# Kernel tuning notes

Hardware: AMD Instinct MI355X
Metric: run time of the kernel (lower is better)

The kernel has to match this reference:

```python
import jax, jax.numpy as jnp
import numpy as np

B, S, D = 2, 2048, 4096
NQ, NKV, DK = 32, 4, 128
GROUPS = NQ // NKV  # 8
NEG = -1e9  # finite stand-in for -inf so fully-masked rows stay NaN-free


def setup_inputs() -> dict:
    key = jax.random.key(0)
    ks = jax.random.split(key, 5)
    return {
        "x": jax.random.normal(ks[0], (B, S, D), jnp.float32),
        "Wq": jax.random.normal(ks[1], (D, NQ * DK), jnp.float32) * 0.02,
        "Wk": jax.random.normal(ks[2], (D, NKV * DK), jnp.float32) * 0.02,
        "Wv": jax.random.normal(ks[3], (D, NKV * DK), jnp.float32) * 0.02,
        "Wo": jax.random.normal(ks[4], (NQ * DK, D), jnp.float32) * 0.02,
    }


def reference(x, Wq, Wk, Wv, Wo):
    b, s, _ = x.shape
    # projections -> [b, heads, s, dk]
    Q = (x @ Wq).reshape(b, s, NQ, DK).transpose(0, 2, 1, 3)
    K = (x @ Wk).reshape(b, s, NKV, DK).transpose(0, 2, 1, 3)
    V = (x @ Wv).reshape(b, s, NKV, DK).transpose(0, 2, 1, 3)
    # GQA: repeat_interleave KV heads to match Q heads
    K = jnp.repeat(K, GROUPS, axis=1)  # [b, NQ, s, dk]
    V = jnp.repeat(V, GROUPS, axis=1)
    scores = jnp.einsum("bhqd,bhkd->bhqk", Q, K) / np.sqrt(DK).astype(np.float32)
    # faithful to source: mask = triu(ones(s, kv_len), diag=kv_len-s+1); fill where mask==0
    mask = jnp.triu(jnp.ones((s, s), jnp.float32), k=1)
    scores = jnp.where(mask == 0, NEG, scores)
    attn = jax.nn.softmax(scores, axis=-1)  # dropout = identity (eval)
    out = jnp.einsum("bhqk,bhkd->bhqd", attn, V)
    out = out.transpose(0, 2, 1, 3).reshape(b, s, NQ * DK)
    return out @ Wo
```

## Files before the change

### kernel.cpp

```cpp
#include <hip/hip_runtime.h>
#include <hip/hip_bf16.h>

#define S_LEN 2048
#define DMODEL 4096
#define NQH 32
#define NKVH 4
#define DKH 128

typedef __attribute__((ext_vector_type(8))) short bf16x8;
typedef __attribute__((ext_vector_type(4))) float f32x4;
typedef __attribute__((ext_vector_type(16))) float f32x16;
typedef __attribute__((ext_vector_type(2))) unsigned u32x2;

union PU { unsigned u[4]; bf16x8 v; };

__device__ __forceinline__ float b2f(short u) {
  union { float f; unsigned int i; } cv;
  cv.i = ((unsigned int)(unsigned short)u) << 16;
  return cv.f;
}

__device__ __forceinline__ unsigned cvt_pk(float lo, float hi) {
  unsigned r;
  asm("v_cvt_pk_bf16_f32 %0, %1, %2" : "=v"(r) : "v"(lo), "v"(hi));
  return r;
}

__device__ __forceinline__ void gload16(const void* g, void* l) {
  __builtin_amdgcn_global_load_lds(
      (const __attribute__((address_space(1))) void*)g,
      (__attribute__((address_space(3))) void*)l, 16, 0, 0);
}

#define BAR()                         \
  {                                   \
    asm volatile("" ::: "memory");    \
    __builtin_amdgcn_s_barrier();     \
    asm volatile("" ::: "memory");    \
  }

__global__ __launch_bounds__(256) void cast_kernel(
    const float* __restrict__ in, __hip_bfloat16* __restrict__ out, int n4) {
  for (int i = blockIdx.x * 256 + threadIdx.x; i < n4; i += gridDim.x * 256) {
    const float4 v = reinterpret_cast<const float4*>(in)[i];
    __hip_bfloat16 t[4] = {__float2bfloat16(v.x), __float2bfloat16(v.y),
                           __float2bfloat16(v.z), __float2bfloat16(v.w)};
    reinterpret_cast<uint2*>(out)[i] = *reinterpret_cast<const uint2*>(t);
  }
}

__device__ __forceinline__ void transpose_tile(const float* __restrict__ W,
                                               __hip_bfloat16* __restrict__ WT,
                                               int K, int N, int n0, int k0,
                                               int tid,
                                               __hip_bfloat16 (*tile)[64]) {
#pragma unroll
  for (int i = 0; i < 2; ++i) {
    const int fid = i * 256 + tid;
    const int r = fid >> 3, cc = fid & 7;
    const float4 v0 = *reinterpret_cast<const float4*>(
        &W[(size_t)(k0 + r) * N + n0 + cc * 8]);
    const float4 v1 = *reinterpret_cast<const float4*>(
        &W[(size_t)(k0 + r) * N + n0 + cc * 8 + 4]);
    __hip_bfloat16 t[8] = {__float2bfloat16(v0.x), __float2bfloat16(v0.y),
                           __float2bfloat16(v0.z), __float2bfloat16(v0.w),
                           __float2bfloat16(v1.x), __float2bfloat16(v1.y),
                           __float2bfloat16(v1.z), __float2bfloat16(v1.w)};
    *reinterpret_cast<bf16x8*>(&tile[r][(cc ^ (r & 7)) << 3]) =
        *reinterpret_cast<const bf16x8*>(t);
  }
  __syncthreads();
  const int n = tid >> 2, kw = tid & 3;
#pragma unroll
  for (int i = 0; i < 2; ++i) {
    const int kc = kw + i * 4;
    __hip_bfloat16 t[8];
#pragma unroll
    for (int j = 0; j < 8; ++j) {
      const int r = kc * 8 + j;
      t[j] = tile[r][((((n >> 3) ^ (r & 7)) << 3)) + (n & 7)];
    }
    *reinterpret_cast<bf16x8*>(&WT[(size_t)(n0 + n) * K + k0 + kc * 8]) =
        *reinterpret_cast<const bf16x8*>(t);
  }
}

__global__ __launch_bounds__(256) void transpose_cast_kernel(
    const float* __restrict__ W, __hip_bfloat16* __restrict__ WT, int K, int N) {
  __shared__ __align__(16) __hip_bfloat16 tile[64][64];
  transpose_tile(W, WT, K, N, blockIdx.x * 64, blockIdx.y * 64, threadIdx.x,
                 tile);
}

__global__ __launch_bounds__(256) void transpose_kv_kernel(
    const float* __restrict__ Wk, const float* __restrict__ Wv,
    __hip_bfloat16* __restrict__ KVT) {
  __shared__ __align__(16) __hip_bfloat16 tile[64][64];
  const int half = blockIdx.x >> 3;
  const float* W = half ? Wv : Wk;
  __hip_bfloat16* WT = KVT + (size_t)half * 512 * 4096;
  transpose_tile(W, WT, 4096, 512, (blockIdx.x & 7) * 64, blockIdx.y * 64,
                 threadIdx.x, tile);
}

template <int WMODE>
__global__ __launch_bounds__(512, 2) void gemm256(
    const __hip_bfloat16* __restrict__ A, const __hip_bfloat16* __restrict__ BT,
    void* __restrict__ C) {
  __shared__ __align__(16) char ldsA[131072];
  const char* lds = &ldsA[0];
  const int tid = threadIdx.x, lane = tid & 63, w = tid >> 6;
  const int l15 = lane & 15, g = lane >> 4;
  const int wr = w >> 2, wcn = w & 3;
  const int id = blockIdx.x;
  const int swz = (id & 7) * 32 + (id >> 3);
  const int bm = (swz >> 4) * 256, bn = (swz & 15) * 256;
  const int row0 = tid >> 3;
  const int kbg = ((tid & 7) * 16) ^ ((row0 & 7) << 4);
  const char* Ab = (const char*)A;
  const char* Bb = (const char*)BT;
  const size_t aR = (size_t)(bm + row0) * 8192 + kbg;
  const size_t bR = (size_t)(bn + row0) * 8192 + kbg;
  char* ldsw = const_cast<char*>(lds) + w * 1024;
  const int sw = (l15 & 7) << 4;
  const int okk = (g * 16) ^ sw;
  const int rA = (wr * 64 + l15) * 128;
  const int rB = (wcn * 32 + l15) * 128;

  f32x4 acc[8][4] = {};

#define STG2(XR, XB, DST)            \
  gload16(XB + (XR), ldsw + (DST));  \
  gload16(XB + (XR) + 524288, ldsw + (DST) + 8192)

  STG2(aR, Ab, 0);
  STG2(bR, Bb, 65536);
  STG2(aR + 1048576, Ab, 16384);
  STG2(bR + 1048576, Bb, 65536 + 16384);
  STG2(aR + 128, Ab, 32768);
  STG2(bR + 128, Bb, 65536 + 32768);

  for (int t = 0; t < 64; ++t) {
    const int pc = t & 1, pn = pc ^ 1;
    const int pA = pc * 32768, pB = 65536 + pc * 32768;
    const size_t s01 = (size_t)((t + 1 < 64) ? t + 1 : t - 1) * 128;
    const size_t s23 = (size_t)((t + 2 < 64) ? t + 2 : t) * 128;
    asm volatile("s_waitcnt vmcnt(4)" ::: "memory");
    BAR();
    bf16x8 a0[4][2], b0[2][2];
#pragma unroll
    for (int m = 0; m < 4; ++m)
#pragma unroll
      for (int kk = 0; kk < 2; ++kk)
        a0[m][kk] = *reinterpret_cast<const bf16x8*>(
            lds + pA + rA + m * 2048 + (okk ^ (kk << 6)));
#pragma unroll
    for (int n = 0; n < 2; ++n)
#pragma unroll
      for (int kk = 0; kk < 2; ++kk)
        b0[n][kk] = *reinterpret_cast<const bf16x8*>(
            lds + pB + rB + n * 2048 + (okk ^ (kk << 6)));
    STG2(aR + 1048576 + s01, Ab, pn * 32768 + 16384);
    __builtin_amdgcn_s_setprio(1);
#pragma unroll
    for (int kk = 0; kk < 2; ++kk)
#pragma unroll
      for (int m = 0; m < 4; ++m)
#pragma unroll
        for (int n = 0; n < 2; ++n)
          acc[m][n] = __builtin_amdgcn_mfma_f32_16x16x32_bf16(
              a0[m][kk], b0[n][kk], acc[m][n], 0, 0, 0);
    __builtin_amdgcn_s_setprio(0);
    bf16x8 b1[2][2];
#pragma unroll
    for (int n = 0; n < 2; ++n)
#pragma unroll
      for (int kk = 0; kk < 2; ++kk)
        b1[n][kk] = *reinterpret_cast<const bf16x8*>(
            lds + pB + 16384 + rB + n * 2048 + (okk ^ (kk << 6)));
    STG2(bR + 1048576 + s01, Bb, 65536 + pn * 32768 + 16384);
    BAR();
    __builtin_amdgcn_s_setprio(1);
#pragma unroll
    for (int kk = 0; kk < 2; ++kk)
#pragma unroll
      for (int m = 0; m < 4; ++m)
#pragma unroll
        for (int n = 0; n < 2; ++n)
          acc[m][2 + n] = __builtin_amdgcn_mfma_f32_16x16x32_bf16(
              a0[m][kk], b1[n][kk], acc[m][2 + n], 0, 0, 0);
    __builtin_amdgcn_s_setprio(0);
    bf16x8 a1[4][2];
#pragma unroll
    for (int m = 0; m < 4; ++m)
#pragma unroll
      for (int kk = 0; kk < 2; ++kk)
        a1[m][kk] = *reinterpret_cast<const bf16x8*>(
            lds + pA + 16384 + rA + m * 2048 + (okk ^ (kk << 6)));
    STG2(aR + s23, Ab, pc * 32768);
    __builtin_amdgcn_s_setprio(1);
#pragma unroll
    for (int kk = 0; kk < 2; ++kk)
#pragma unroll
      for (int m = 0; m < 4; ++m)
#pragma unroll
        for (int n = 0; n < 2; ++n)
          acc[4 + m][n] = __builtin_amdgcn_mfma_f32_16x16x32_bf16(
              a1[m][kk], b0[n][kk], acc[4 + m][n], 0, 0, 0);
    __builtin_amdgcn_s_setprio(0);
    STG2(bR + s23, Bb, 65536 + pc * 32768);
    __builtin_amdgcn_s_setprio(1);
#pragma unroll
    for (int kk = 0; kk < 2; ++kk)
#pragma unroll
      for (int m = 0; m < 4; ++m)
#pragma unroll
        for (int n = 0; n < 2; ++n)
          acc[4 + m][2 + n] = __builtin_amdgcn_mfma_f32_16x16x32_bf16(
              a1[m][kk], b1[n][kk], acc[4 + m][2 + n], 0, 0, 0);
    __builtin_amdgcn_s_setprio(0);
  }
  asm volatile("s_waitcnt vmcnt(0)" ::: "memory");

  const int crow0 = bm + wr * 64 + g * 4;
  const int ccol0 = bn + wcn * 32 + l15;
#pragma unroll
  for (int M = 0; M < 8; ++M)
#pragma unroll
    for (int N = 0; N < 4; ++N) {
      const int row = crow0 + (M >> 2) * 128 + (M & 3) * 16;
      const int col = ccol0 + (N >> 1) * 128 + (N & 1) * 16;
#pragma unroll
      for (int r = 0; r < 4; ++r) {
        if constexpr (WMODE == 0)
          ((float*)C)[(size_t)(row + r) * 4096 + col] = acc[M][N][r];
        else
          ((__hip_bfloat16*)C)[(size_t)(row + r) * 4096 + col] =
              __float2bfloat16(acc[M][N][r]);
      }
    }
}

__global__ __launch_bounds__(256) void gemm_kv(
    const __hip_bfloat16* __restrict__ A, const __hip_bfloat16* __restrict__ BT,
    __hip_bfloat16* __restrict__ Kb, __hip_bfloat16* __restrict__ VT) {
  __shared__ __align__(16) char ldsb[3][12288];
  char* ldsbase = &ldsb[0][0];
  const int tid = threadIdx.x, lane = tid & 63, w = tid >> 6;
  const int l15 = lane & 15, l4 = lane >> 4;
  const int bm = blockIdx.y * 64, bn = blockIdx.x * 128;
  const int wr = (w >> 1) * 32, wc = (w & 1) * 64;
  const int srow = lane >> 2, scol = (lane & 3) * 8;
  const char* ga = (const char*)&A[(size_t)(bm + (tid >> 2)) * 4096 + scol];
  const char* gb =
      (const char*)&BT[(size_t)(bn + w * 16 + srow) * 4096 + scol];
  f32x4 acc[2][4] = {};

#define KVSTG(T, BUF)                                                   \
  {                                                                     \
    const size_t ko = (size_t)(T) * 64;                                 \
    gload16(ga + ko, ldsbase + (BUF) * 12288 + w * 1024);               \
    gload16(gb + ko, ldsbase + (BUF) * 12288 + 4096 + w * 1024);        \
    gload16(gb + 524288 + ko, ldsbase + (BUF) * 12288 + 8192 + w * 1024); \
  }

  KVSTG(0, 0);
  KVSTG(1, 1);
  int cur = 0;
  for (int t = 0; t < 128; ++t) {
    asm volatile("s_waitcnt vmcnt(3)" ::: "memory");
    BAR();
    const char* bp = ldsbase + cur * 12288;
    bf16x8 af[2], bfr[4];
#pragma unroll
    for (int m = 0; m < 2; ++m)
      af[m] = *reinterpret_cast<const bf16x8*>(
          bp + (wr + m * 16 + l15) * 64 + l4 * 16);
#pragma unroll
    for (int n = 0; n < 4; ++n)
      bfr[n] = *reinterpret_cast<const bf16x8*>(
          bp + 4096 + (wc + n * 16 + l15) * 64 + l4 * 16);
    const int t2 = (t + 2 < 128) ? t + 2 : t;
    int b2 = cur + 2;
    if (b2 >= 3) b2 -= 3;
    KVSTG(t2, b2);
#pragma unroll
    for (int m = 0; m < 2; ++m)
#pragma unroll
      for (int n = 0; n < 4; ++n)
        acc[m][n] = __builtin_amdgcn_mfma_f32_16x16x32_bf16(af[m], bfr[n],
                                                            acc[m][n], 0, 0, 0);
    ++cur;
    if (cur == 3) cur = 0;
  }
  asm volatile("s_waitcnt vmcnt(0)" ::: "memory");

#pragma unroll
  for (int m = 0; m < 2; ++m)
#pragma unroll
    for (int n = 0; n < 4; ++n) {
      const int row = bm + wr + m * 16 + l4 * 4;
      const int col = bn + wc + n * 16 + l15;
      if (col < 512) {
#pragma unroll
        for (int r = 0; r < 4; ++r)
          Kb[(size_t)(row + r) * 512 + col] = __float2bfloat16(acc[m][n][r]);
      } else {
        const int b = row >> 11, s = row & 2047;
        uint2 st;
        st.x = cvt_pk(acc[m][n][0], acc[m][n][1]);
        st.y = cvt_pk(acc[m][n][2], acc[m][n][3]);
        *reinterpret_cast<uint2*>(
            &VT[(size_t)(b * 512 + (col - 512)) * 2048 + s]) = st;
      }
    }
}

__global__ __launch_bounds__(512, 2) void attn_kernel(
    const __hip_bfloat16* __restrict__ Q, const __hip_bfloat16* __restrict__ Kb,
    const __hip_bfloat16* __restrict__ VT, __hip_bfloat16* __restrict__ O) {
  __shared__ __align__(16) __hip_bfloat16 Kbuf[2][64 * 128];
  __shared__ __align__(16) __hip_bfloat16 Vbuf[2][128 * 64];
  const int tid = threadIdx.x, lane = tid & 63, w = tid >> 6;
  const int l31 = lane & 31, h = lane >> 5;
  const int d = blockIdx.x;
  const int xg = d & 7, hh = (d >> 3) & 7, pr = d >> 6;
  const int bh = xg * 8 + hh;
  const int b = bh >> 5, hq = bh & 31, kvh = (bh & 31) >> 3;
  const char* kbase = (const char*)Kb + (size_t)(b * S_LEN) * 1024 + kvh * 256;
  const char* vbase = (const char*)VT + (size_t)(b * 512 + kvh * 128) * 4096;
  const __hip_bfloat16* qbase =
      Q + (size_t)(b * S_LEN) * DMODEL + (size_t)hq * DKH;
  __hip_bfloat16* obase = O + (size_t)(b * S_LEN) * DMODEL + (size_t)hq * DKH;
  const int krr = lane >> 4, kcb = (lane & 15) * 16;
  const int vrr = lane >> 3, vcb = (lane & 7) * 16;
  char* klds = (char*)&Kbuf[0][0] + w * 2048;
  char* vlds = (char*)&Vbuf[0][0] + w * 2048;
  const int swr = (lane & 7) * 16;
  const float SCL2 = 0.12751742f;

  int par = 0;
  for (int ph = 0; ph < 2; ++ph) {
    const int pp = ph ? (7 - pr) : pr;
    const int qw = pp * 256 + w * 32;
    const int qa = qw + l31;
    bf16x8 qf[8];
#pragma unroll
    for (int dkb = 0; dkb < 8; ++dkb)
      qf[dkb] = *reinterpret_cast<const bf16x8*>(
          &qbase[(size_t)qa * DMODEL + dkb * 16 + h * 8]);
    float lsum = 0.f;
    f32x16 oaccT[4] = {};
    const int t0 = pp * 4;
    {
      const int kv0 = t0 * 64;
#pragma unroll
      for (int i = 0; i < 2; ++i) {
        const int rr = 8 * w + 4 * i + krr;
        gload16(kbase + (size_t)(kv0 + rr) * 1024 + (kcb ^ ((rr & 7) * 16)),
                klds + par * 16384 + i * 1024);
        const int r2 = 16 * w + 8 * i + vrr;
        gload16(vbase + (size_t)r2 * 4096 + kv0 * 2 + (vcb ^ ((r2 & 7) * 16)),
                vlds + par * 16384 + i * 1024);
      }
    }
    for (int t = t0; t < 32; ++t) {
      __syncthreads();
      if (t + 1 < 32) {
        const int kv0 = (t + 1) * 64;
        const int np = par ^ 1;
#pragma unroll
        for (int i = 0; i < 2; ++i) {
          const int rr = 8 * w + 4 * i + krr;
          gload16(kbase + (size_t)(kv0 + rr) * 1024 + (kcb ^ ((rr & 7) * 16)),
                  klds + np * 16384 + i * 1024);
          const int r2 = 16 * w + 8 * i + vrr;
          gload16(vbase + (size_t)r2 * 4096 + kv0 * 2 + (vcb ^ ((r2 & 7) * 16)),
                  vlds + np * 16384 + i * 1024);
        }
      }
      const char* kp = (const char*)&Kbuf[0][0] + par * 16384;
      const char* vp = (const char*)&Vbuf[0][0] + par * 16384;
#pragma unroll
      for (int kvb = 0; kvb < 2; ++kvb) {
        f32x16 s = {};
#pragma unroll
        for (int dkb = 0; dkb < 8; ++dkb) {
          const bf16x8 kf = *reinterpret_cast<const bf16x8*>(
              kp + (kvb * 32 + l31) * 256 + ((dkb * 32 + h * 16) ^ swr));
          s = __builtin_amdgcn_mfma_f32_32x32x16_bf16(kf, qf[dkb], s, 0, 0, 0);
        }
#pragma unroll
        for (int r = 0; r < 16; ++r)
          s[r] = __builtin_amdgcn_exp2f(fmaf(s[r], SCL2, -16.f));
        if (t * 64 < qw + 32) {
#pragma unroll
          for (int r = 0; r < 16; ++r) {
            const int kvl = (r & 3) + 8 * (r >> 2) + 4 * h;
            if (t * 64 + kvb * 32 + kvl <= qa) s[r] = 0.f;
          }
        }
#pragma unroll
        for (int r = 0; r < 16; ++r) lsum += s[r];
        unsigned wv[8];
#pragma unroll
        for (int i = 0; i < 8; ++i) wv[i] = cvt_pk(s[2 * i], s[2 * i + 1]);
        const u32x2 s02 =
            __builtin_amdgcn_permlane32_swap(wv[0], wv[2], false, false);
        const u32x2 s13 =
            __builtin_amdgcn_permlane32_swap(wv[1], wv[3], false, false);
        const u32x2 s46 =
            __builtin_amdgcn_permlane32_swap(wv[4], wv[6], false, false);
        const u32x2 s57 =
            __builtin_amdgcn_permlane32_swap(wv[5], wv[7], false, false);
        PU pb1, pb2;
        pb1.u[0] = s02[0]; pb1.u[1] = s13[0]; pb1.u[2] = s02[1]; pb1.u[3] = s13[1];
        pb2.u[0] = s46[0]; pb2.u[1] = s57[0]; pb2.u[2] = s46[1]; pb2.u[3] = s57[1];
#pragma unroll
        for (int dkblk = 0; dkblk < 4; ++dkblk) {
          const bf16x8 vf1 = *reinterpret_cast<const bf16x8*>(
              vp + (dkblk * 32 + l31) * 128 + ((kvb * 64 + h * 16) ^ swr));
          oaccT[dkblk] = __builtin_amdgcn_mfma_f32_32x32x16_bf16(
              vf1, pb1.v, oaccT[dkblk], 0, 0, 0);
          const bf16x8 vf2 = *reinterpret_cast<const bf16x8*>(
              vp + (dkblk * 32 + l31) * 128 + ((kvb * 64 + 32 + h * 16) ^ swr));
          oaccT[dkblk] = __builtin_amdgcn_mfma_f32_32x32x16_bf16(
              vf2, pb2.v, oaccT[dkblk], 0, 0, 0);
        }
      }
      par ^= 1;
    }
    lsum += __shfl_xor(lsum, 32);
    const float rinv = 1.f / lsum;
    __hip_bfloat16* orow = obase + (size_t)qa * DMODEL;
#pragma unroll
    for (int dkblk = 0; dkblk < 4; ++dkblk)
#pragma unroll
      for (int b4 = 0; b4 < 4; ++b4) {
        uint2 st;
        st.x = cvt_pk(oaccT[dkblk][4 * b4 + 0] * rinv,
                      oaccT[dkblk][4 * b4 + 1] * rinv);
        st.y = cvt_pk(oaccT[dkblk][4 * b4 + 2] * rinv,
                      oaccT[dkblk][4 * b4 + 3] * rinv);
        *reinterpret_cast<uint2*>(&orow[dkblk * 32 + b4 * 8 + 4 * h]) = st;
      }
    __syncthreads();
  }
}

__global__ __launch_bounds__(128) void fixup_kernel(
    const __hip_bfloat16* __restrict__ VT, __hip_bfloat16* __restrict__ O) {
  const int b = blockIdx.x >> 5;
  const int h = blockIdx.x & 31;
  const int kvh = h >> 3;
  const int dk = threadIdx.x;
  const __hip_bfloat16* row = &VT[(size_t)(b * 512 + kvh * DKH + dk) * S_LEN];
  float s = 0.f;
  for (int i = 0; i < S_LEN / 8; ++i) {
    const bf16x8 v = *reinterpret_cast<const bf16x8*>(&row[i * 8]);
#pragma unroll
    for (int j = 0; j < 8; ++j) s += b2f(v[j]);
  }
  O[(size_t)(b * S_LEN + S_LEN - 1) * DMODEL + h * DKH + dk] =
      __float2bfloat16(s * (1.f / S_LEN));
}

extern "C" void kernel_launch(void* const* d_in, const int* in_sizes, int n_in,
                              void* d_out, int out_size, void* d_ws,
                              size_t ws_size, hipStream_t stream) {
  (void)in_sizes; (void)n_in; (void)out_size; (void)ws_size;
  const float* x = (const float*)d_in[0];
  const float* Wq = (const float*)d_in[1];
  const float* Wk = (const float*)d_in[2];
  const float* Wv = (const float*)d_in[3];
  const float* Wo = (const float*)d_in[4];
  float* out = (float*)d_out;

  char* ws = (char*)d_ws;
  __hip_bfloat16* xb  = (__hip_bfloat16*)(ws + 0);
  __hip_bfloat16* WT0 = (__hip_bfloat16*)(ws + 33554432ull);
  __hip_bfloat16* KVT = (__hip_bfloat16*)(ws + 67108864ull);
  __hip_bfloat16* Qb  = (__hip_bfloat16*)(ws + 75497472ull);
  __hip_bfloat16* Kb  = (__hip_bfloat16*)(ws + 109051904ull);
  __hip_bfloat16* VT  = (__hip_bfloat16*)(ws + 113246208ull);
  __hip_bfloat16* AO  = xb;

  const int M = 2 * S_LEN;
  dim3 blk(256);

  cast_kernel<<<dim3(2048), blk, 0, stream>>>(x, xb, (M * DMODEL) / 4);
  transpose_cast_kernel<<<dim3(64, 64), blk, 0, stream>>>(Wq, WT0, DMODEL, DMODEL);
  gemm256<1><<<dim3(256), dim3(512), 0, stream>>>(xb, WT0, Qb);
  transpose_kv_kernel<<<dim3(16, 64), blk, 0, stream>>>(Wk, Wv, KVT);
  gemm_kv<<<dim3(8, 64), blk, 0, stream>>>(xb, KVT, Kb, VT);
  attn_kernel<<<dim3(256), dim3(512), 0, stream>>>(Qb, Kb, VT, AO);
  fixup_kernel<<<dim3(64), dim3(128), 0, stream>>>(VT, AO);
  transpose_cast_kernel<<<dim3(64, 64), blk, 0, stream>>>(Wo, WT0, DMODEL, DMODEL);
  gemm256<0><<<dim3(256), dim3(512), 0, stream>>>(AO, WT0, out);
}
```

Before: 428.2 us.

## Software-pipeline attention: overlap PV of previous tile with QK of current tile

Measured after the change: 432.8 us. About the same (+1.1%).

```diff
diff --git a/kernel.cpp b/kernel.cpp
--- a/kernel.cpp
+++ b/kernel.cpp
@@ -320,7 +320,7 @@
     const __hip_bfloat16* __restrict__ Q, const __hip_bfloat16* __restrict__ Kb,
     const __hip_bfloat16* __restrict__ VT, __hip_bfloat16* __restrict__ O) {
   __shared__ __align__(16) __hip_bfloat16 Kbuf[2][64 * 128];
-  __shared__ __align__(16) __hip_bfloat16 Vbuf[2][128 * 64];
+  __shared__ __align__(16) __hip_bfloat16 Vbuf[3][128 * 64];
   const int tid = threadIdx.x, lane = tid & 63, w = tid >> 6;
   const int l31 = lane & 31, h = lane >> 5;
   const int d = blockIdx.x;
@@ -339,7 +339,21 @@
   const int swr = (lane & 7) * 16;
   const float SCL2 = 0.12751742f;
 
-  int par = 0;
+#define ASTG(T)                                                              \
+  {                                                                          \
+    const int kv0_ = (T) * 64;                                               \
+    const int kbi_ = (T) & 1;                                                \
+    int vbi_ = (T) % 3;                                                      \
+    _Pragma("unroll") for (int i = 0; i < 2; ++i) {                          \
+      const int rr = 8 * w + 4 * i + krr;                                    \
+      gload16(kbase + (size_t)(kv0_ + rr) * 1024 + (kcb ^ ((rr & 7) * 16)),  \
+              klds + kbi_ * 16384 + i * 1024);                               \
+      const int r2 = 16 * w + 8 * i + vrr;                                   \
+      gload16(vbase + (size_t)r2 * 4096 + kv0_ * 2 + (vcb ^ ((r2 & 7) * 16)),\
+              vlds + vbi_ * 16384 + i * 1024);                               \
+    }                                                                        \
+  }
+
   for (int ph = 0; ph < 2; ++ph) {
     const int pp = ph ? (7 - pr) : pr;
     const int qw = pp * 256 + w * 32;
@@ -351,36 +365,14 @@
           &qbase[(size_t)qa * DMODEL + dkb * 16 + h * 8]);
     float lsum = 0.f;
     f32x16 oaccT[4] = {};
+    PU opb[2][2];
     const int t0 = pp * 4;
-    {
-      const int kv0 = t0 * 64;
-#pragma unroll
-      for (int i = 0; i < 2; ++i) {
-        const int rr = 8 * w + 4 * i + krr;
-        gload16(kbase + (size_t)(kv0 + rr) * 1024 + (kcb ^ ((rr & 7) * 16)),
-                klds + par * 16384 + i * 1024);
-        const int r2 = 16 * w + 8 * i + vrr;
-        gload16(vbase + (size_t)r2 * 4096 + kv0 * 2 + (vcb ^ ((r2 & 7) * 16)),
-                vlds + par * 16384 + i * 1024);
-      }
-    }
+    ASTG(t0);
     for (int t = t0; t < 32; ++t) {
       __syncthreads();
-      if (t + 1 < 32) {
-        const int kv0 = (t + 1) * 64;
-        const int np = par ^ 1;
-#pragma unroll
-        for (int i = 0; i < 2; ++i) {
-          const int rr = 8 * w + 4 * i + krr;
-          gload16(kbase + (size_t)(kv0 + rr) * 1024 + (kcb ^ ((rr & 7) * 16)),
-                  klds + np * 16384 + i * 1024);
-          const int r2 = 16 * w + 8 * i + vrr;
-          gload16(vbase + (size_t)r2 * 4096 + kv0 * 2 + (vcb ^ ((r2 & 7) * 16)),
-                  vlds + np * 16384 + i * 1024);
-        }
-      }
-      const char* kp = (const char*)&Kbuf[0][0] + par * 16384;
-      const char* vp = (const char*)&Vbuf[0][0] + par * 16384;
+      if (t + 1 < 32) ASTG(t + 1);
+      const char* kp = (const char*)&Kbuf[0][0] + (t & 1) * 16384;
+      PU npb[2][2];
 #pragma unroll
       for (int kvb = 0; kvb < 2; ++kvb) {
         f32x16 s = {};
@@ -413,22 +405,51 @@
             __builtin_amdgcn_permlane32_swap(wv[4], wv[6], false, false);
         const u32x2 s57 =
             __builtin_amdgcn_permlane32_swap(wv[5], wv[7], false, false);
-        PU pb1, pb2;
-        pb1.u[0] = s02[0]; pb1.u[1] = s13[0]; pb1.u[2] = s02[1]; pb1.u[3] = s13[1];
-        pb2.u[0] = s46[0]; pb2.u[1] = s57[0]; pb2.u[2] = s46[1]; pb2.u[3] = s57[1];
+        npb[kvb][0].u[0] = s02[0]; npb[kvb][0].u[1] = s13[0];
+        npb[kvb][0].u[2] = s02[1]; npb[kvb][0].u[3] = s13[1];
+        npb[kvb][1].u[0] = s46[0]; npb[kvb][1].u[1] = s57[0];
+        npb[kvb][1].u[2] = s46[1]; npb[kvb][1].u[3] = s57[1];
+      }
+      if (t > t0) {
+        const char* vpo =
+            (const char*)&Vbuf[0][0] + ((t - 1) % 3) * 16384;
+#pragma unroll
+        for (int kvb = 0; kvb < 2; ++kvb)
+#pragma unroll
+          for (int dkblk = 0; dkblk < 4; ++dkblk) {
+            const bf16x8 vf1 = *reinterpret_cast<const bf16x8*>(
+                vpo + (dkblk * 32 + l31) * 128 + ((kvb * 64 + h * 16) ^ swr));
+            oaccT[dkblk] = __builtin_amdgcn_mfma_f32_32x32x16_bf16(
+                vf1, opb[kvb][0].v, oaccT[dkblk], 0, 0, 0);
+            const bf16x8 vf2 = *reinterpret_cast<const bf16x8*>(
+                vpo + (dkblk * 32 + l31) * 128 +
+                ((kvb * 64 + 32 + h * 16) ^ swr));
+            oaccT[dkblk] = __builtin_amdgcn_mfma_f32_32x32x16_bf16(
+                vf2, opb[kvb][1].v, oaccT[dkblk], 0, 0, 0);
+          }
+      }
+#pragma unroll
+      for (int kvb = 0; kvb < 2; ++kvb) {
+        opb[kvb][0] = npb[kvb][0];
+        opb[kvb][1] = npb[kvb][1];
+      }
+    }
+    {
+      const char* vpo = (const char*)&Vbuf[0][0] + (31 % 3) * 16384;
+#pragma unroll
+      for (int kvb = 0; kvb < 2; ++kvb)
 #pragma unroll
         for (int dkblk = 0; dkblk < 4; ++dkblk) {
           const bf16x8 vf1 = *reinterpret_cast<const bf16x8*>(
-              vp + (dkblk * 32 + l31) * 128 + ((kvb * 64 + h * 16) ^ swr));
+              vpo + (dkblk * 32 + l31) * 128 + ((kvb * 64 + h * 16) ^ swr));
           oaccT[dkblk] = __builtin_amdgcn_mfma_f32_32x32x16_bf16(
-              vf1, pb1.v, oaccT[dkblk], 0, 0, 0);
+              vf1, opb[kvb][0].v, oaccT[dkblk], 0, 0, 0);
           const bf16x8 vf2 = *reinterpret_cast<const bf16x8*>(
-              vp + (dkblk * 32 + l31) * 128 + ((kvb * 64 + 32 + h * 16) ^ swr));
+              vpo + (dkblk * 32 + l31) * 128 +
+              ((kvb * 64 + 32 + h * 16) ^ swr));
           oaccT[dkblk] = __builtin_amdgcn_mfma_f32_32x32x16_bf16(
-              vf2, pb2.v, oaccT[dkblk], 0, 0, 0);
+              vf2, opb[kvb][1].v, oaccT[dkblk], 0, 0, 0);
         }
-      }
-      par ^= 1;
     }
     lsum += __shfl_xor(lsum, 32);
     const float rinv = 1.f / lsum;
```
